# Performance work log

Hardware: AMD Instinct MI355X
Metric: run time of the kernel (lower is better)

Reference implementation:

```python
import jax, jax.numpy as jnp
import numpy as np

N = 100000
E = 6400000
H = 64  # hidden_nf


def setup_inputs() -> dict:
    key = jax.random.key(0)
    ks = jax.random.split(key, 12)
    x = jax.random.normal(ks[0], (N, 3), dtype=jnp.float32)
    vel = jax.random.normal(ks[1], (N, 3), dtype=jnp.float32)
    vel_norm = jax.random.uniform(ks[2], (N, 1), dtype=jnp.float32)
    edge_index = jax.random.randint(ks[3], (2, E), 0, N, dtype=jnp.int32)
    # coord_mlp_vel: Linear(1,H) -> LeakyReLU(0.2) -> Linear(H,1)
    W1 = jax.random.normal(ks[4], (H, 1), dtype=jnp.float32) * (1.0 / np.sqrt(1))
    b1 = jnp.zeros((H,), dtype=jnp.float32)
    W2 = jax.random.normal(ks[5], (1, H), dtype=jnp.float32) * (1.0 / np.sqrt(H))
    b2 = jnp.zeros((1,), dtype=jnp.float32)
    # phi: Linear(1,H) -> LeakyReLU(0.2) -> Linear(H,1,bias=False, xavier gain=0.001) -> Tanh
    Wp1 = jax.random.normal(ks[6], (H, 1), dtype=jnp.float32) * (1.0 / np.sqrt(1))
    bp1 = jnp.zeros((H,), dtype=jnp.float32)
    Wp2 = jax.random.normal(ks[7], (1, H), dtype=jnp.float32) * 0.001
    return {"x": x, "vel_norm": vel_norm, "vel": vel, "edge_index": edge_index,
            "W1": W1, "b1": b1, "W2": W2, "b2": b2,
            "Wp1": Wp1, "bp1": bp1, "Wp2": Wp2}


def reference(x, vel_norm, vel, edge_index, W1, b1, W2, b2, Wp1, bp1, Wp2):
    row, col = edge_index[0], edge_index[1]
    # edge_model: gather endpoint positions, radial distance -> tiny MLP -> scaled diff
    x_diff = x[row] - x[col]                                   # [E, 3]
    radial = jnp.sqrt(jnp.sum(x_diff * x_diff, axis=1, keepdims=True))  # [E, 1]
    h = jax.nn.leaky_relu(radial @ Wp1.T + bp1, 0.2)           # [E, H]
    e_out = jnp.tanh(h @ Wp2.T)                                # [E, 1]
    m_ij = x_diff * e_out                                      # [E, 3]
    # node_model: unsorted_segment_mean over row
    agg_sum = jax.ops.segment_sum(m_ij, row, num_segments=x.shape[0])           # [N, 3]
    cnt = jax.ops.segment_sum(jnp.ones((m_ij.shape[0], 1), m_ij.dtype), row,
                              num_segments=x.shape[0])                           # [N, 1]
    x_out = x + agg_sum / jnp.maximum(cnt, 1.0)
    # velocity term: x + vel * coord_mlp_vel(vel_norm)
    hv = jax.nn.leaky_relu(vel_norm @ W1.T + b1, 0.2)          # [N, H]
    scale = hv @ W2.T + b2                                     # [N, 1]
    return x_out + vel * scale
```

## Files before the change

kernel.cpp:

```cpp
#include <hip/hip_runtime.h>
#include <hip/hip_fp16.h>
#include <math.h>

#define LEAKY 0.2f
#define HDIM 64
#define EPB 4096
#define TPB1 256
#define PERT (EPB / TPB1)
#define RANGE 1024
#define RSH 10
#define KMAX 128
#define NSUB 4
#define NSLICE 8
#define FS2 262144.0f
#define INVFS2 (1.0f / 262144.0f)
#define FBIAS 4194304


__device__ __forceinline__ float fast_tanh(float v) {
    float e = __builtin_amdgcn_exp2f(v * 2.88539008178f);
    return 1.0f - 2.0f * __builtin_amdgcn_rcpf(e + 1.0f);
}

__device__ __forceinline__ float edge_eo(float rad, float C, bool slow,
                                         const float* sW1, const float* sb1,
                                         const float* sW2) {
    if (!slow) return fast_tanh(C * rad);
    float a = 0.f;
    #pragma unroll
    for (int k = 0; k < HDIM; k++) {
        float h = fmaf(rad, sW1[k], sb1[k]);
        h = (h > 0.f) ? h : LEAKY * h;
        a = fmaf(sW2[k], h, a);
    }
    return fast_tanh(a);
}

__global__ void repack_h_kernel(const float* __restrict__ x, uint2* __restrict__ xh, int N,
                                const float* __restrict__ Wp1, const float* __restrict__ bp1,
                                const float* __restrict__ Wp2, float* __restrict__ consts,
                                uint4* __restrict__ acc4, unsigned* __restrict__ cursor, int K) {
    int i = blockIdx.x * blockDim.x + threadIdx.x;
    if (i < N) {
        unsigned hx = __half_as_ushort(__float2half(x[3*i]));
        unsigned hy = __half_as_ushort(__float2half(x[3*i+1]));
        unsigned hz = __half_as_ushort(__float2half(x[3*i+2]));
        xh[i] = make_uint2((hy << 16) | hx, hz);
        acc4[i] = make_uint4(0u, 0u, 0u, 0u);
    }
    if (blockIdx.x == 0) {
        if (threadIdx.x < 64) {
            int k = threadIdx.x;
            float w1 = Wp1[k];
            float slope = (w1 >= 0.f) ? 1.f : LEAKY;
            float c = Wp2[k] * w1 * slope;
            float bnz = (bp1[k] != 0.f) ? 1.f : 0.f;
            #pragma unroll
            for (int off = 32; off > 0; off >>= 1) {
                c += __shfl_down(c, off, 64);
                bnz += __shfl_down(bnz, off, 64);
            }
            if (k == 0) { consts[0] = c; consts[1] = bnz; }
        }
        for (int k = threadIdx.x; k < NSUB * K; k += 256) cursor[k] = 0u;
    }
}

__device__ __forceinline__ unsigned long long pack_rec(float dx, float dy, float dz,
                                                       float eo, unsigned lid) {
    unsigned hx = __half_as_ushort(__float2half(dx * eo));
    unsigned hy = __half_as_ushort(__float2half(dy * eo));
    unsigned hz = __half_as_ushort(__float2half(dz * eo));
    return (unsigned long long)lid
         | ((unsigned long long)hx << 11)
         | ((unsigned long long)hy << 27)
         | ((unsigned long long)hz << 43);
}

__device__ __forceinline__ uint2 make_record(uint2 ga, uint2 gb, int r,
                                             float C, bool slow,
                                             const float* sW1, const float* sb1,
                                             const float* sW2) {
    float ax = __half2float(__ushort_as_half((unsigned short)(ga.x & 0xFFFF)));
    float ay = __half2float(__ushort_as_half((unsigned short)(ga.x >> 16)));
    float az = __half2float(__ushort_as_half((unsigned short)(ga.y & 0xFFFF)));
    float bx = __half2float(__ushort_as_half((unsigned short)(gb.x & 0xFFFF)));
    float by = __half2float(__ushort_as_half((unsigned short)(gb.x >> 16)));
    float bz = __half2float(__ushort_as_half((unsigned short)(gb.y & 0xFFFF)));
    float dx = ax - bx, dy = ay - by, dz = az - bz;
    float rad = sqrtf(dx*dx + dy*dy + dz*dz);
    float eo = edge_eo(rad, C, slow, sW1, sb1, sW2);
    unsigned long long u = pack_rec(dx, dy, dz, eo, (unsigned)r & (RANGE - 1));
    return make_uint2((unsigned)u, (unsigned)(u >> 32));
}

__device__ __forceinline__ void rec_to_acc4(uint2 r, unsigned b_, unsigned* acc4) {
    unsigned long long u = ((unsigned long long)r.y << 32) | r.x;
    unsigned lid = (unsigned)(u & (RANGE - 1));
    unsigned node = b_ * RANGE + lid;
    float mx = __half2float(__ushort_as_half((unsigned short)((u >> 11) & 0xFFFF)));
    float my = __half2float(__ushort_as_half((unsigned short)((u >> 27) & 0xFFFF)));
    float mz = __half2float(__ushort_as_half((unsigned short)((u >> 43) & 0xFFFF)));
    atomicAdd(&acc4[4*node + 0], (unsigned)__float2int_rn(mx * FS2));
    atomicAdd(&acc4[4*node + 1], (unsigned)__float2int_rn(my * FS2));
    atomicAdd(&acc4[4*node + 2], (unsigned)__float2int_rn(mz * FS2));
    atomicAdd(&acc4[4*node + 3], 1u);
}

__global__ __launch_bounds__(TPB1) void fused5_kernel(
        const uint2* __restrict__ xh,
        const int* __restrict__ ei,
        const float* __restrict__ Wp1, const float* __restrict__ bp1,
        const float* __restrict__ Wp2, const float* __restrict__ consts,
        unsigned* __restrict__ cursor, unsigned* __restrict__ acc4,
        uint2* __restrict__ recs, int E, int K, unsigned csub) {
    __shared__ uint2 stage[EPB];
    __shared__ unsigned char bucket_of[EPB];
    __shared__ unsigned hist[KMAX];
    __shared__ unsigned scanv[KMAX + 1];
    __shared__ unsigned cur[KMAX];
    __shared__ unsigned gstart[KMAX];
    __shared__ float sW1[HDIM], sb1[HDIM], sW2[HDIM];
    const float C = consts[0];
    const bool slow = (consts[1] != 0.f);
    const unsigned sub = (unsigned)blockIdx.x & (NSUB - 1);
    if (slow) {
        for (int k = threadIdx.x; k < HDIM; k += TPB1) {
            sW1[k] = Wp1[k]; sb1[k] = bp1[k]; sW2[k] = Wp2[k];
        }
    }
    for (int k = threadIdx.x; k < K; k += TPB1) hist[k] = 0;
    __syncthreads();

    const size_t base = (size_t)blockIdx.x * EPB;
    const unsigned t = threadIdx.x;
    uint2 rc[PERT];
    unsigned bk[PERT];
    if (base + EPB <= (size_t)E && (E & 3) == 0) {
        const int4* pr = (const int4*)(ei + base);
        const int4* pc = (const int4*)(ei + (size_t)E + base);
        int4 rv0 = pr[t];
        int4 rv1 = pr[t + TPB1];
        int4 rv2 = pr[t + 2 * TPB1];
        int4 rv3 = pr[t + 3 * TPB1];
        int4 cv0 = pc[t];
        int4 cv1 = pc[t + TPB1];
        int4 cv2 = pc[t + 2 * TPB1];
        int4 cv3 = pc[t + 3 * TPB1];
        {
            uint2 ga0 = xh[rv0.x], ga1 = xh[rv0.y], ga2 = xh[rv0.z], ga3 = xh[rv0.w];
            uint2 ga4 = xh[rv1.x], ga5 = xh[rv1.y], ga6 = xh[rv1.z], ga7 = xh[rv1.w];
            uint2 gb0 = xh[cv0.x], gb1 = xh[cv0.y], gb2 = xh[cv0.z], gb3 = xh[cv0.w];
            uint2 gb4 = xh[cv1.x], gb5 = xh[cv1.y], gb6 = xh[cv1.z], gb7 = xh[cv1.w];
            rc[0] = make_record(ga0, gb0, rv0.x, C, slow, sW1, sb1, sW2);
            rc[1] = make_record(ga1, gb1, rv0.y, C, slow, sW1, sb1, sW2);
            rc[2] = make_record(ga2, gb2, rv0.z, C, slow, sW1, sb1, sW2);
            rc[3] = make_record(ga3, gb3, rv0.w, C, slow, sW1, sb1, sW2);
            rc[4] = make_record(ga4, gb4, rv1.x, C, slow, sW1, sb1, sW2);
            rc[5] = make_record(ga5, gb5, rv1.y, C, slow, sW1, sb1, sW2);
            rc[6] = make_record(ga6, gb6, rv1.z, C, slow, sW1, sb1, sW2);
            rc[7] = make_record(ga7, gb7, rv1.w, C, slow, sW1, sb1, sW2);
        }
        {
            uint2 ga0 = xh[rv2.x], ga1 = xh[rv2.y], ga2 = xh[rv2.z], ga3 = xh[rv2.w];
            uint2 ga4 = xh[rv3.x], ga5 = xh[rv3.y], ga6 = xh[rv3.z], ga7 = xh[rv3.w];
            uint2 gb0 = xh[cv2.x], gb1 = xh[cv2.y], gb2 = xh[cv2.z], gb3 = xh[cv2.w];
            uint2 gb4 = xh[cv3.x], gb5 = xh[cv3.y], gb6 = xh[cv3.z], gb7 = xh[cv3.w];
            rc[8]  = make_record(ga0, gb0, rv2.x, C, slow, sW1, sb1, sW2);
            rc[9]  = make_record(ga1, gb1, rv2.y, C, slow, sW1, sb1, sW2);
            rc[10] = make_record(ga2, gb2, rv2.z, C, slow, sW1, sb1, sW2);
            rc[11] = make_record(ga3, gb3, rv2.w, C, slow, sW1, sb1, sW2);
            rc[12] = make_record(ga4, gb4, rv3.x, C, slow, sW1, sb1, sW2);
            rc[13] = make_record(ga5, gb5, rv3.y, C, slow, sW1, sb1, sW2);
            rc[14] = make_record(ga6, gb6, rv3.z, C, slow, sW1, sb1, sW2);
            rc[15] = make_record(ga7, gb7, rv3.w, C, slow, sW1, sb1, sW2);
        }
        bk[0]  = (unsigned)rv0.x >> RSH; bk[1]  = (unsigned)rv0.y >> RSH;
        bk[2]  = (unsigned)rv0.z >> RSH; bk[3]  = (unsigned)rv0.w >> RSH;
        bk[4]  = (unsigned)rv1.x >> RSH; bk[5]  = (unsigned)rv1.y >> RSH;
        bk[6]  = (unsigned)rv1.z >> RSH; bk[7]  = (unsigned)rv1.w >> RSH;
        bk[8]  = (unsigned)rv2.x >> RSH; bk[9]  = (unsigned)rv2.y >> RSH;
        bk[10] = (unsigned)rv2.z >> RSH; bk[11] = (unsigned)rv2.w >> RSH;
        bk[12] = (unsigned)rv3.x >> RSH; bk[13] = (unsigned)rv3.y >> RSH;
        bk[14] = (unsigned)rv3.z >> RSH; bk[15] = (unsigned)rv3.w >> RSH;
        #pragma unroll
        for (int i = 0; i < PERT; i++) atomicAdd(&hist[bk[i]], 1u);
    } else {
        #pragma unroll
        for (int i = 0; i < PERT; i++) {
            size_t e = base + (size_t)i * TPB1 + t;
            bk[i] = 0xFFFFFFFFu;
            if (e < (size_t)E) {
                int r = ei[e];
                int c = ei[(size_t)E + e];
                uint2 ga = xh[r], gb = xh[c];
                rc[i] = make_record(ga, gb, r, C, slow, sW1, sb1, sW2);
                bk[i] = (unsigned)r >> RSH;
                atomicAdd(&hist[bk[i]], 1u);
            }
        }
    }
    __syncthreads();
    unsigned res = 0;
    if (t < (unsigned)K) {
        unsigned myc = hist[t];
        if (myc) res = atomicAdd(&cursor[t * NSUB + sub], myc);
    }
    if (t >= 192) {
        int l = t - 192;
        unsigned origA = (l < K) ? hist[l] : 0u;
        unsigned origB = (l + 64 < K) ? hist[l + 64] : 0u;
        unsigned a = origA, b = origB;
        #pragma unroll
        for (int off = 1; off < 64; off <<= 1) {
            unsigned va = __shfl_up(a, off, 64);
            unsigned vb = __shfl_up(b, off, 64);
            if (l >= off) { a += va; b += vb; }
        }
        unsigned totA = __shfl(a, 63, 64);
        unsigned grand = totA + __shfl(b, 63, 64);
        unsigned exA = a - origA;
        unsigned exB = totA + b - origB;
        scanv[l] = exA;  cur[l] = exA;
        scanv[l + 64] = exB;  cur[l + 64] = exB;
        if (l == 63) scanv[K] = grand;
    }
    __syncthreads();
    #pragma unroll
    for (int i = 0; i < PERT; i++) {
        if (bk[i] != 0xFFFFFFFFu) {
            unsigned slot = atomicAdd(&cur[bk[i]], 1u);
            stage[slot] = rc[i];
            bucket_of[slot] = (unsigned char)bk[i];
        }
    }
    if (t < (unsigned)K) gstart[t] = res;
    __syncthreads();
    unsigned total = scanv[K];
    for (unsigned j = t; j < total; j += TPB1) {
        unsigned b_ = bucket_of[j];
        unsigned off = gstart[b_] + (j - scanv[b_]);
        if (off < csub) recs[(size_t)(b_ * NSUB + sub) * csub + off] = stage[j];
        else            rec_to_acc4(stage[j], b_, acc4);
    }
}

__device__ __forceinline__ void proc_rec2(unsigned lo, unsigned hi,
                                          unsigned long long* accA,
                                          unsigned long long* accB) {
    unsigned long long u = ((unsigned long long)hi << 32) | lo;
    unsigned lid = (unsigned)(u & (RANGE - 1));
    float mx = __half2float(__ushort_as_half((unsigned short)((u >> 11) & 0xFFFF)));
    float my = __half2float(__ushort_as_half((unsigned short)((u >> 27) & 0xFFFF)));
    float mz = __half2float(__ushort_as_half((unsigned short)((u >> 43) & 0xFFFF)));
    unsigned ix = (unsigned)(__float2int_rn(mx * FS2) + FBIAS);
    unsigned iy = (unsigned)(__float2int_rn(my * FS2) + FBIAS);
    unsigned iz = (unsigned)(__float2int_rn(mz * FS2) + FBIAS);
    atomicAdd(&accA[lid], ((unsigned long long)ix << 32) | (unsigned long long)iy);
    atomicAdd(&accB[lid], ((unsigned long long)iz << 32) | 1ull);
}

__global__ __launch_bounds__(256) void reduce5_kernel(
        const uint2* __restrict__ recs, const unsigned* __restrict__ cursor,
        uint4* __restrict__ slices, int N, int K, unsigned csub) {
    __shared__ unsigned long long accA[RANGE];
    __shared__ unsigned long long accB[RANGE];
    const int b = blockIdx.x / NSLICE;
    const int s = blockIdx.x % NSLICE;
    const int r = s & (NSUB - 1);
    const int p = s / NSUB;
    for (int i = threadIdx.x; i < RANGE; i += 256) { accA[i] = 0ull; accB[i] = 0ull; }
    __syncthreads();
    unsigned cnt = cursor[b * NSUB + r];
    if (cnt > csub) cnt = csub;
    unsigned pairs = (cnt + 1) >> 1;
    unsigned perp = (pairs + 1) >> 1;
    unsigned p0 = (unsigned)p * perp;
    unsigned p1 = p0 + perp; if (p1 > pairs) p1 = pairs;
    const uint4* rb4 = (const uint4*)(recs + (size_t)(b * NSUB + r) * csub);
    unsigned j = p0 + threadIdx.x;
    if (p0 < p1) {
        while (j + 256 < p1) {
            uint4 v0 = rb4[j];
            uint4 v1 = rb4[j + 256];
            proc_rec2(v0.x, v0.y, accA, accB);
            if (2*j + 1 < cnt) proc_rec2(v0.z, v0.w, accA, accB);
            proc_rec2(v1.x, v1.y, accA, accB);
            if (2*(j+256) + 1 < cnt) proc_rec2(v1.z, v1.w, accA, accB);
            j += 512;
        }
        while (j < p1) {
            uint4 v = rb4[j];
            proc_rec2(v.x, v.y, accA, accB);
            if (2*j + 1 < cnt) proc_rec2(v.z, v.w, accA, accB);
            j += 256;
        }
    }
    __syncthreads();
    const int nbase = b * RANGE;
    for (int i = threadIdx.x; i < RANGE; i += 256) {
        int node = nbase + i;
        if (node < N) {
            unsigned long long A = accA[i], B = accB[i];
            slices[(size_t)s * N + node] =
                make_uint4((unsigned)(A >> 32), (unsigned)A,
                           (unsigned)(B >> 32), (unsigned)B);
        }
    }
}

__global__ void node_merge_kernel(const float* __restrict__ x,
                                  const float* __restrict__ vel_norm,
                                  const float* __restrict__ vel,
                                  const float* __restrict__ W1, const float* __restrict__ b1,
                                  const float* __restrict__ W2, const float* __restrict__ b2,
                                  const uint4* __restrict__ slices,
                                  const uint4* __restrict__ acc4,
                                  float* __restrict__ out, int N) {
    __shared__ float sW1[HDIM], sb1[HDIM], sW2[HDIM];
    for (int k = threadIdx.x; k < HDIM; k += blockDim.x) {
        sW1[k] = W1[k]; sb1[k] = b1[k]; sW2[k] = W2[k];
    }
    __syncthreads();
    int i = blockIdx.x * blockDim.x + threadIdx.x;
    if (i >= N) return;
    unsigned long long sxb = 0, syb = 0, szb = 0;
    unsigned sc = 0;
    #pragma unroll
    for (int s = 0; s < NSLICE; s++) {
        uint4 v = slices[(size_t)s * N + i];
        sxb += v.x; syb += v.y; szb += v.z; sc += v.w;
    }
    uint4 a4 = acc4[i];
    long long fx = (long long)sxb - (long long)sc * (long long)FBIAS + (long long)(int)a4.x;
    long long fy = (long long)syb - (long long)sc * (long long)FBIAS + (long long)(int)a4.y;
    long long fz = (long long)szb - (long long)sc * (long long)FBIAS + (long long)(int)a4.z;
    float cntf = (float)(sc + a4.w);
    float sx = (float)fx * INVFS2;
    float sy = (float)fy * INVFS2;
    float sz = (float)fz * INVFS2;
    float vn = vel_norm[i];
    float a = b2[0];
    #pragma unroll
    for (int k = 0; k < HDIM; k++) {
        float h = fmaf(vn, sW1[k], sb1[k]);
        h = (h > 0.f) ? h : LEAKY * h;
        a = fmaf(sW2[k], h, a);
    }
    float inv = 1.0f / fmaxf(cntf, 1.0f);
    out[3*i]     = x[3*i]     + sx * inv + vel[3*i]     * a;
    out[3*i + 1] = x[3*i + 1] + sy * inv + vel[3*i + 1] * a;
    out[3*i + 2] = x[3*i + 2] + sz * inv + vel[3*i + 2] * a;
}

__global__ void precompute_kernel(const float* __restrict__ Wp1,
                                  const float* __restrict__ bp1,
                                  const float* __restrict__ Wp2,
                                  float* __restrict__ consts) {
    int k = threadIdx.x;
    float w1 = Wp1[k];
    float slope = (w1 >= 0.f) ? 1.f : LEAKY;
    float c = Wp2[k] * w1 * slope;
    float bnz = (bp1[k] != 0.f) ? 1.f : 0.f;
    #pragma unroll
    for (int off = 32; off > 0; off >>= 1) {
        c += __shfl_down(c, off, 64);
        bnz += __shfl_down(bnz, off, 64);
    }
    if (k == 0) { consts[0] = c; consts[1] = bnz; }
}

__global__ void edge_atomic_kernel(const float* __restrict__ x, const int* __restrict__ ei,
                                   const float* __restrict__ Wp1, const float* __restrict__ bp1,
                                   const float* __restrict__ Wp2, const float* __restrict__ consts,
                                   float* __restrict__ acc, int E) {
    __shared__ float sW1[HDIM], sb1[HDIM], sW2[HDIM];
    const float C = consts[0];
    const bool slow = (consts[1] != 0.f);
    if (slow) {
        for (int k = threadIdx.x; k < HDIM; k += blockDim.x) {
            sW1[k] = Wp1[k]; sb1[k] = bp1[k]; sW2[k] = Wp2[k];
        }
        __syncthreads();
    }
    int e = blockIdx.x * blockDim.x + threadIdx.x;
    if (e >= E) return;
    int r = ei[e];
    int c = ei[E + e];
    float dx = x[3*r] - x[3*c];
    float dy = x[3*r+1] - x[3*c+1];
    float dz = x[3*r+2] - x[3*c+2];
    float rad = sqrtf(dx*dx + dy*dy + dz*dz);
    float eo = edge_eo(rad, C, slow, sW1, sb1, sW2);
    float* basep = acc + ((size_t)r << 2);
    atomicAdd(basep + 0, dx * eo);
    atomicAdd(basep + 1, dy * eo);
    atomicAdd(basep + 2, dz * eo);
    atomicAdd(basep + 3, 1.f);
}

__global__ void node_kernel(const float* __restrict__ x, const float* __restrict__ vel_norm,
                            const float* __restrict__ vel,
                            const float* __restrict__ W1, const float* __restrict__ b1,
                            const float* __restrict__ W2, const float* __restrict__ b2,
                            const float4* __restrict__ slices,
                            float* __restrict__ out, int N, int S) {
    __shared__ float sW1[HDIM], sb1[HDIM], sW2[HDIM];
    for (int k = threadIdx.x; k < HDIM; k += blockDim.x) {
        sW1[k] = W1[k]; sb1[k] = b1[k]; sW2[k] = W2[k];
    }
    __syncthreads();
    int i = blockIdx.x * blockDim.x + threadIdx.x;
    if (i >= N) return;
    float sx = 0.f, sy = 0.f, sz = 0.f, sc = 0.f;
    for (int s = 0; s < S; s++) {
        float4 v = slices[(size_t)s * N + i];
        sx += v.x; sy += v.y; sz += v.z; sc += v.w;
    }
    float vn = vel_norm[i];
    float a = b2[0];
    #pragma unroll
    for (int k = 0; k < HDIM; k++) {
        float h = fmaf(vn, sW1[k], sb1[k]);
        h = (h > 0.f) ? h : LEAKY * h;
        a = fmaf(sW2[k], h, a);
    }
    float inv = 1.0f / fmaxf(sc, 1.0f);
    out[3*i]     = x[3*i]     + sx * inv + vel[3*i]     * a;
    out[3*i + 1] = x[3*i + 1] + sy * inv + vel[3*i + 1] * a;
    out[3*i + 2] = x[3*i + 2] + sz * inv + vel[3*i + 2] * a;
}

extern "C" void kernel_launch(void* const* d_in, const int* in_sizes, int n_in,
                              void* d_out, int out_size, void* d_ws, size_t ws_size,
                              hipStream_t stream) {
    const float* x        = (const float*)d_in[0];
    const float* vel_norm = (const float*)d_in[1];
    const float* vel      = (const float*)d_in[2];
    const int*   ei       = (const int*)  d_in[3];
    const float* W1       = (const float*)d_in[4];
    const float* b1       = (const float*)d_in[5];
    const float* W2       = (const float*)d_in[6];
    const float* b2       = (const float*)d_in[7];
    const float* Wp1      = (const float*)d_in[8];
    const float* bp1      = (const float*)d_in[9];
    const float* Wp2      = (const float*)d_in[10];

    const int N = in_sizes[0] / 3;
    const int E = in_sizes[3] / 2;
    const int K = (N + RANGE - 1) / RANGE;
    const int nblk = (E + EPB - 1) / EPB;

    unsigned csub = (unsigned)(E / (K * NSUB)) + 1024u;
    csub = (csub + 63u) & ~63u;

    size_t rec_bytes = (size_t)K * NSUB * csub * sizeof(uint2);
    size_t sp_slices = rec_bytes;
    size_t sp_xh     = sp_slices + (size_t)NSLICE * N * sizeof(uint4);
    size_t sp_acc    = (sp_xh + (size_t)N * sizeof(uint2) + 15) & ~(size_t)15;
    size_t sp_cur    = sp_acc + (size_t)N * sizeof(uint4);
    size_t sp_const  = (sp_cur + (size_t)NSUB * KMAX * sizeof(unsigned) + 15) & ~(size_t)15;
    size_t need      = sp_const + 32;

    if (K <= KMAX && ws_size >= need) {
        uint2*    recs   = (uint2*)   d_ws;
        uint4*    slices = (uint4*)   ((char*)d_ws + sp_slices);
        uint2*    xh     = (uint2*)   ((char*)d_ws + sp_xh);
        unsigned* acc4   = (unsigned*)((char*)d_ws + sp_acc);
        unsigned* cursor = (unsigned*)((char*)d_ws + sp_cur);
        float*    consts = (float*)   ((char*)d_ws + sp_const);

        repack_h_kernel<<<(N + 255) / 256, 256, 0, stream>>>(
            x, xh, N, Wp1, bp1, Wp2, consts, (uint4*)acc4, cursor, K);
        fused5_kernel<<<nblk, TPB1, 0, stream>>>(
            xh, ei, Wp1, bp1, Wp2, consts, cursor, acc4, recs, E, K, csub);
        reduce5_kernel<<<K * NSLICE, 256, 0, stream>>>(recs, cursor, slices, N, K, csub);
        node_merge_kernel<<<(N + 255) / 256, 256, 0, stream>>>(
            x, vel_norm, vel, W1, b1, W2, b2, slices, (const uint4*)acc4,
            (float*)d_out, N);
    } else {
        float* acc    = (float*)d_ws;
        float* consts = (float*)((char*)d_ws + (size_t)N * sizeof(float4));
        hipMemsetAsync(d_ws, 0, (size_t)N * sizeof(float4) + 32, stream);
        precompute_kernel<<<1, 64, 0, stream>>>(Wp1, bp1, Wp2, consts);
        edge_atomic_kernel<<<(E + 255) / 256, 256, 0, stream>>>(x, ei, Wp1, bp1, Wp2,
                                                                consts, acc, E);
        node_kernel<<<(N + 255) / 256, 256, 0, stream>>>(x, vel_norm, vel, W1, b1, W2, b2,
                                                         (const float4*)acc, (float*)d_out, N, 1);
    }
}
```

Before: 185.8 us.

## Scatter edge records directly to global buckets, dropping LDS staging and scan

New measurement: 198.3 us. 6.7% more time.

```diff
diff --git a/kernel.cpp b/kernel.cpp
--- a/kernel.cpp
+++ b/kernel.cpp
@@ -4,7 +4,7 @@
 
 #define LEAKY 0.2f
 #define HDIM 64
-#define EPB 4096
+#define EPB 2048
 #define TPB1 256
 #define PERT (EPB / TPB1)
 #define RANGE 1024
@@ -107,18 +107,15 @@
     atomicAdd(&acc4[4*node + 3], 1u);
 }
 
-__global__ __launch_bounds__(TPB1) void fused5_kernel(
+__global__ __launch_bounds__(TPB1, 6) void fused6_kernel(
         const uint2* __restrict__ xh,
         const int* __restrict__ ei,
         const float* __restrict__ Wp1, const float* __restrict__ bp1,
         const float* __restrict__ Wp2, const float* __restrict__ consts,
         unsigned* __restrict__ cursor, unsigned* __restrict__ acc4,
         uint2* __restrict__ recs, int E, int K, unsigned csub) {
-    __shared__ uint2 stage[EPB];
-    __shared__ unsigned char bucket_of[EPB];
     __shared__ unsigned hist[KMAX];
-    __shared__ unsigned scanv[KMAX + 1];
-    __shared__ unsigned cur[KMAX];
+    __shared__ unsigned curk[KMAX];
     __shared__ unsigned gstart[KMAX];
     __shared__ float sW1[HDIM], sb1[HDIM], sW2[HDIM];
     const float C = consts[0];
@@ -129,7 +126,7 @@
             sW1[k] = Wp1[k]; sb1[k] = bp1[k]; sW2[k] = Wp2[k];
         }
     }
-    for (int k = threadIdx.x; k < K; k += TPB1) hist[k] = 0;
+    for (int k = threadIdx.x; k < K; k += TPB1) { hist[k] = 0; curk[k] = 0; }
     __syncthreads();
 
     const size_t base = (size_t)blockIdx.x * EPB;
@@ -141,48 +138,24 @@
         const int4* pc = (const int4*)(ei + (size_t)E + base);
         int4 rv0 = pr[t];
         int4 rv1 = pr[t + TPB1];
-        int4 rv2 = pr[t + 2 * TPB1];
-        int4 rv3 = pr[t + 3 * TPB1];
         int4 cv0 = pc[t];
         int4 cv1 = pc[t + TPB1];
-        int4 cv2 = pc[t + 2 * TPB1];
-        int4 cv3 = pc[t + 3 * TPB1];
-        {
-            uint2 ga0 = xh[rv0.x], ga1 = xh[rv0.y], ga2 = xh[rv0.z], ga3 = xh[rv0.w];
-            uint2 ga4 = xh[rv1.x], ga5 = xh[rv1.y], ga6 = xh[rv1.z], ga7 = xh[rv1.w];
-            uint2 gb0 = xh[cv0.x], gb1 = xh[cv0.y], gb2 = xh[cv0.z], gb3 = xh[cv0.w];
-            uint2 gb4 = xh[cv1.x], gb5 = xh[cv1.y], gb6 = xh[cv1.z], gb7 = xh[cv1.w];
-            rc[0] = make_record(ga0, gb0, rv0.x, C, slow, sW1, sb1, sW2);
-            rc[1] = make_record(ga1, gb1, rv0.y, C, slow, sW1, sb1, sW2);
-            rc[2] = make_record(ga2, gb2, rv0.z, C, slow, sW1, sb1, sW2);
-            rc[3] = make_record(ga3, gb3, rv0.w, C, slow, sW1, sb1, sW2);
-            rc[4] = make_record(ga4, gb4, rv1.x, C, slow, sW1, sb1, sW2);
-            rc[5] = make_record(ga5, gb5, rv1.y, C, slow, sW1, sb1, sW2);
-            rc[6] = make_record(ga6, gb6, rv1.z, C, slow, sW1, sb1, sW2);
-            rc[7] = make_record(ga7, gb7, rv1.w, C, slow, sW1, sb1, sW2);
-        }
-        {
-            uint2 ga0 = xh[rv2.x], ga1 = xh[rv2.y], ga2 = xh[rv2.z], ga3 = xh[rv2.w];
-            uint2 ga4 = xh[rv3.x], ga5 = xh[rv3.y], ga6 = xh[rv3.z], ga7 = xh[rv3.w];
-            uint2 gb0 = xh[cv2.x], gb1 = xh[cv2.y], gb2 = xh[cv2.z], gb3 = xh[cv2.w];
-            uint2 gb4 = xh[cv3.x], gb5 = xh[cv3.y], gb6 = xh[cv3.z], gb7 = xh[cv3.w];
-            rc[8]  = make_record(ga0, gb0, rv2.x, C, slow, sW1, sb1, sW2);
-            rc[9]  = make_record(ga1, gb1, rv2.y, C, slow, sW1, sb1, sW2);
-            rc[10] = make_record(ga2, gb2, rv2.z, C, slow, sW1, sb1, sW2);
-            rc[11] = make_record(ga3, gb3, rv2.w, C, slow, sW1, sb1, sW2);
-            rc[12] = make_record(ga4, gb4, rv3.x, C, slow, sW1, sb1, sW2);
-            rc[13] = make_record(ga5, gb5, rv3.y, C, slow, sW1, sb1, sW2);
-            rc[14] = make_record(ga6, gb6, rv3.z, C, slow, sW1, sb1, sW2);
-            rc[15] = make_record(ga7, gb7, rv3.w, C, slow, sW1, sb1, sW2);
-        }
-        bk[0]  = (unsigned)rv0.x >> RSH; bk[1]  = (unsigned)rv0.y >> RSH;
-        bk[2]  = (unsigned)rv0.z >> RSH; bk[3]  = (unsigned)rv0.w >> RSH;
-        bk[4]  = (unsigned)rv1.x >> RSH; bk[5]  = (unsigned)rv1.y >> RSH;
-        bk[6]  = (unsigned)rv1.z >> RSH; bk[7]  = (unsigned)rv1.w >> RSH;
-        bk[8]  = (unsigned)rv2.x >> RSH; bk[9]  = (unsigned)rv2.y >> RSH;
-        bk[10] = (unsigned)rv2.z >> RSH; bk[11] = (unsigned)rv2.w >> RSH;
-        bk[12] = (unsigned)rv3.x >> RSH; bk[13] = (unsigned)rv3.y >> RSH;
-        bk[14] = (unsigned)rv3.z >> RSH; bk[15] = (unsigned)rv3.w >> RSH;
+        uint2 ga0 = xh[rv0.x], ga1 = xh[rv0.y], ga2 = xh[rv0.z], ga3 = xh[rv0.w];
+        uint2 ga4 = xh[rv1.x], ga5 = xh[rv1.y], ga6 = xh[rv1.z], ga7 = xh[rv1.w];
+        uint2 gb0 = xh[cv0.x], gb1 = xh[cv0.y], gb2 = xh[cv0.z], gb3 = xh[cv0.w];
+        uint2 gb4 = xh[cv1.x], gb5 = xh[cv1.y], gb6 = xh[cv1.z], gb7 = xh[cv1.w];
+        rc[0] = make_record(ga0, gb0, rv0.x, C, slow, sW1, sb1, sW2);
+        rc[1] = make_record(ga1, gb1, rv0.y, C, slow, sW1, sb1, sW2);
+        rc[2] = make_record(ga2, gb2, rv0.z, C, slow, sW1, sb1, sW2);
+        rc[3] = make_record(ga3, gb3, rv0.w, C, slow, sW1, sb1, sW2);
+        rc[4] = make_record(ga4, gb4, rv1.x, C, slow, sW1, sb1, sW2);
+        rc[5] = make_record(ga5, gb5, rv1.y, C, slow, sW1, sb1, sW2);
+        rc[6] = make_record(ga6, gb6, rv1.z, C, slow, sW1, sb1, sW2);
+        rc[7] = make_record(ga7, gb7, rv1.w, C, slow, sW1, sb1, sW2);
+        bk[0] = (unsigned)rv0.x >> RSH; bk[1] = (unsigned)rv0.y >> RSH;
+        bk[2] = (unsigned)rv0.z >> RSH; bk[3] = (unsigned)rv0.w >> RSH;
+        bk[4] = (unsigned)rv1.x >> RSH; bk[5] = (unsigned)rv1.y >> RSH;
+        bk[6] = (unsigned)rv1.z >> RSH; bk[7] = (unsigned)rv1.w >> RSH;
         #pragma unroll
         for (int i = 0; i < PERT; i++) atomicAdd(&hist[bk[i]], 1u);
     } else {
@@ -201,47 +174,19 @@
         }
     }
     __syncthreads();
-    unsigned res = 0;
     if (t < (unsigned)K) {
         unsigned myc = hist[t];
-        if (myc) res = atomicAdd(&cursor[t * NSUB + sub], myc);
-    }
-    if (t >= 192) {
-        int l = t - 192;
-        unsigned origA = (l < K) ? hist[l] : 0u;
-        unsigned origB = (l + 64 < K) ? hist[l + 64] : 0u;
-        unsigned a = origA, b = origB;
-        #pragma unroll
-        for (int off = 1; off < 64; off <<= 1) {
-            unsigned va = __shfl_up(a, off, 64);
-            unsigned vb = __shfl_up(b, off, 64);
-            if (l >= off) { a += va; b += vb; }
-        }
-        unsigned totA = __shfl(a, 63, 64);
-        unsigned grand = totA + __shfl(b, 63, 64);
-        unsigned exA = a - origA;
-        unsigned exB = totA + b - origB;
-        scanv[l] = exA;  cur[l] = exA;
-        scanv[l + 64] = exB;  cur[l + 64] = exB;
-        if (l == 63) scanv[K] = grand;
+        gstart[t] = myc ? atomicAdd(&cursor[t * NSUB + sub], myc) : 0u;
     }
     __syncthreads();
     #pragma unroll
     for (int i = 0; i < PERT; i++) {
         if (bk[i] != 0xFFFFFFFFu) {
-            unsigned slot = atomicAdd(&cur[bk[i]], 1u);
-            stage[slot] = rc[i];
-            bucket_of[slot] = (unsigned char)bk[i];
-        }
-    }
-    if (t < (unsigned)K) gstart[t] = res;
-    __syncthreads();
-    unsigned total = scanv[K];
-    for (unsigned j = t; j < total; j += TPB1) {
-        unsigned b_ = bucket_of[j];
-        unsigned off = gstart[b_] + (j - scanv[b_]);
-        if (off < csub) recs[(size_t)(b_ * NSUB + sub) * csub + off] = stage[j];
-        else            rec_to_acc4(stage[j], b_, acc4);
+            unsigned r = atomicAdd(&curk[bk[i]], 1u);
+            unsigned off = gstart[bk[i]] + r;
+            if (off < csub) recs[(size_t)(bk[i] * NSUB + sub) * csub + off] = rc[i];
+            else            rec_to_acc4(rc[i], bk[i], acc4);
+        }
     }
 }
 
@@ -472,7 +417,7 @@
 
         repack_h_kernel<<<(N + 255) / 256, 256, 0, stream>>>(
             x, xh, N, Wp1, bp1, Wp2, consts, (uint4*)acc4, cursor, K);
-        fused5_kernel<<<nblk, TPB1, 0, stream>>>(
+        fused6_kernel<<<nblk, TPB1, 0, stream>>>(
             xh, ei, Wp1, bp1, Wp2, consts, cursor, acc4, recs, E, K, csub);
         reduce5_kernel<<<K * NSLICE, 256, 0, stream>>>(recs, cursor, slices, N, K, csub);
         node_merge_kernel<<<(N + 255) / 256, 256, 0, stream>>>(
```

## Fuse segment reduction with node update into one kernel per range

Applied to the files above, without the earlier changes.

After: 186.9 us. Within noise of the previous version (+0.6%).

```diff
diff --git a/kernel.cpp b/kernel.cpp
--- a/kernel.cpp
+++ b/kernel.cpp
@@ -11,7 +11,6 @@
 #define RSH 10
 #define KMAX 128
 #define NSUB 4
-#define NSLICE 8
 #define FS2 262144.0f
 #define INVFS2 (1.0f / 262144.0f)
 #define FBIAS 4194304
@@ -260,97 +259,65 @@
     atomicAdd(&accB[lid], ((unsigned long long)iz << 32) | 1ull);
 }
 
-__global__ __launch_bounds__(256) void reduce5_kernel(
+__global__ __launch_bounds__(1024) void reduce_node_kernel(
         const uint2* __restrict__ recs, const unsigned* __restrict__ cursor,
-        uint4* __restrict__ slices, int N, int K, unsigned csub) {
+        const float* __restrict__ x, const float* __restrict__ vel_norm,
+        const float* __restrict__ vel,
+        const float* __restrict__ W1, const float* __restrict__ b1,
+        const float* __restrict__ W2, const float* __restrict__ b2,
+        const uint4* __restrict__ acc4,
+        float* __restrict__ out, int N, unsigned csub) {
     __shared__ unsigned long long accA[RANGE];
     __shared__ unsigned long long accB[RANGE];
-    const int b = blockIdx.x / NSLICE;
-    const int s = blockIdx.x % NSLICE;
-    const int r = s & (NSUB - 1);
-    const int p = s / NSUB;
-    for (int i = threadIdx.x; i < RANGE; i += 256) { accA[i] = 0ull; accB[i] = 0ull; }
-    __syncthreads();
-    unsigned cnt = cursor[b * NSUB + r];
-    if (cnt > csub) cnt = csub;
-    unsigned pairs = (cnt + 1) >> 1;
-    unsigned perp = (pairs + 1) >> 1;
-    unsigned p0 = (unsigned)p * perp;
-    unsigned p1 = p0 + perp; if (p1 > pairs) p1 = pairs;
-    const uint4* rb4 = (const uint4*)(recs + (size_t)(b * NSUB + r) * csub);
-    unsigned j = p0 + threadIdx.x;
-    if (p0 < p1) {
-        while (j + 256 < p1) {
-            uint4 v0 = rb4[j];
-            uint4 v1 = rb4[j + 256];
-            proc_rec2(v0.x, v0.y, accA, accB);
-            if (2*j + 1 < cnt) proc_rec2(v0.z, v0.w, accA, accB);
-            proc_rec2(v1.x, v1.y, accA, accB);
-            if (2*(j+256) + 1 < cnt) proc_rec2(v1.z, v1.w, accA, accB);
-            j += 512;
-        }
-        while (j < p1) {
+    __shared__ float sW1[HDIM], sb1[HDIM], sW2[HDIM];
+    const int b = blockIdx.x;
+    const unsigned t = threadIdx.x;
+    if (t < HDIM) { sW1[t] = W1[t]; sb1[t] = b1[t]; sW2[t] = W2[t]; }
+    accA[t] = 0ull; accB[t] = 0ull;
+    __syncthreads();
+    #pragma unroll
+    for (int r = 0; r < NSUB; r++) {
+        unsigned cnt = cursor[b * NSUB + r];
+        if (cnt > csub) cnt = csub;
+        const uint2* rb = recs + (size_t)(b * NSUB + r) * csub;
+        const uint4* rb4 = (const uint4*)rb;
+        unsigned pairs = cnt >> 1;
+        for (unsigned j = t; j < pairs; j += 1024) {
             uint4 v = rb4[j];
             proc_rec2(v.x, v.y, accA, accB);
-            if (2*j + 1 < cnt) proc_rec2(v.z, v.w, accA, accB);
-            j += 256;
-        }
-    }
-    __syncthreads();
-    const int nbase = b * RANGE;
-    for (int i = threadIdx.x; i < RANGE; i += 256) {
-        int node = nbase + i;
-        if (node < N) {
-            unsigned long long A = accA[i], B = accB[i];
-            slices[(size_t)s * N + node] =
-                make_uint4((unsigned)(A >> 32), (unsigned)A,
-                           (unsigned)(B >> 32), (unsigned)B);
-        }
-    }
-}
-
-__global__ void node_merge_kernel(const float* __restrict__ x,
-                                  const float* __restrict__ vel_norm,
-                                  const float* __restrict__ vel,
-                                  const float* __restrict__ W1, const float* __restrict__ b1,
-                                  const float* __restrict__ W2, const float* __restrict__ b2,
-                                  const uint4* __restrict__ slices,
-                                  const uint4* __restrict__ acc4,
-                                  float* __restrict__ out, int N) {
-    __shared__ float sW1[HDIM], sb1[HDIM], sW2[HDIM];
-    for (int k = threadIdx.x; k < HDIM; k += blockDim.x) {
-        sW1[k] = W1[k]; sb1[k] = b1[k]; sW2[k] = W2[k];
-    }
-    __syncthreads();
-    int i = blockIdx.x * blockDim.x + threadIdx.x;
-    if (i >= N) return;
-    unsigned long long sxb = 0, syb = 0, szb = 0;
-    unsigned sc = 0;
-    #pragma unroll
-    for (int s = 0; s < NSLICE; s++) {
-        uint4 v = slices[(size_t)s * N + i];
-        sxb += v.x; syb += v.y; szb += v.z; sc += v.w;
-    }
-    uint4 a4 = acc4[i];
-    long long fx = (long long)sxb - (long long)sc * (long long)FBIAS + (long long)(int)a4.x;
-    long long fy = (long long)syb - (long long)sc * (long long)FBIAS + (long long)(int)a4.y;
-    long long fz = (long long)szb - (long long)sc * (long long)FBIAS + (long long)(int)a4.z;
-    float cntf = (float)(sc + a4.w);
-    float sx = (float)fx * INVFS2;
-    float sy = (float)fy * INVFS2;
-    float sz = (float)fz * INVFS2;
-    float vn = vel_norm[i];
-    float a = b2[0];
-    #pragma unroll
-    for (int k = 0; k < HDIM; k++) {
-        float h = fmaf(vn, sW1[k], sb1[k]);
-        h = (h > 0.f) ? h : LEAKY * h;
-        a = fmaf(sW2[k], h, a);
-    }
-    float inv = 1.0f / fmaxf(cntf, 1.0f);
-    out[3*i]     = x[3*i]     + sx * inv + vel[3*i]     * a;
-    out[3*i + 1] = x[3*i + 1] + sy * inv + vel[3*i + 1] * a;
-    out[3*i + 2] = x[3*i + 2] + sz * inv + vel[3*i + 2] * a;
+            proc_rec2(v.z, v.w, accA, accB);
+        }
+        if ((cnt & 1u) && t == 0) {
+            uint2 last = rb[cnt - 1];
+            proc_rec2(last.x, last.y, accA, accB);
+        }
+    }
+    __syncthreads();
+    int node = b * RANGE + (int)t;
+    if (node < N) {
+        unsigned long long A = accA[t], B = accB[t];
+        unsigned sc = (unsigned)B;
+        uint4 a4 = acc4[node];
+        long long fx = (long long)(A >> 32) - (long long)sc * (long long)FBIAS + (long long)(int)a4.x;
+        long long fy = (long long)(unsigned)A - (long long)sc * (long long)FBIAS + (long long)(int)a4.y;
+        long long fz = (long long)(B >> 32) - (long long)sc * (long long)FBIAS + (long long)(int)a4.z;
+        float cntf = (float)(sc + a4.w);
+        float sx = (float)fx * INVFS2;
+        float sy = (float)fy * INVFS2;
+        float sz = (float)fz * INVFS2;
+        float vn = vel_norm[node];
+        float a = b2[0];
+        #pragma unroll
+        for (int k = 0; k < HDIM; k++) {
+            float h = fmaf(vn, sW1[k], sb1[k]);
+            h = (h > 0.f) ? h : LEAKY * h;
+            a = fmaf(sW2[k], h, a);
+        }
+        float inv = 1.0f / fmaxf(cntf, 1.0f);
+        out[3*node]     = x[3*node]     + sx * inv + vel[3*node]     * a;
+        out[3*node + 1] = x[3*node + 1] + sy * inv + vel[3*node + 1] * a;
+        out[3*node + 2] = x[3*node + 2] + sz * inv + vel[3*node + 2] * a;
+    }
 }
 
 __global__ void precompute_kernel(const float* __restrict__ Wp1,
@@ -455,8 +422,7 @@
     csub = (csub + 63u) & ~63u;
 
     size_t rec_bytes = (size_t)K * NSUB * csub * sizeof(uint2);
-    size_t sp_slices = rec_bytes;
-    size_t sp_xh     = sp_slices + (size_t)NSLICE * N * sizeof(uint4);
+    size_t sp_xh     = rec_bytes;
     size_t sp_acc    = (sp_xh + (size_t)N * sizeof(uint2) + 15) & ~(size_t)15;
     size_t sp_cur    = sp_acc + (size_t)N * sizeof(uint4);
     size_t sp_const  = (sp_cur + (size_t)NSUB * KMAX * sizeof(unsigned) + 15) & ~(size_t)15;
@@ -464,7 +430,6 @@
 
     if (K <= KMAX && ws_size >= need) {
         uint2*    recs   = (uint2*)   d_ws;
-        uint4*    slices = (uint4*)   ((char*)d_ws + sp_slices);
         uint2*    xh     = (uint2*)   ((char*)d_ws + sp_xh);
         unsigned* acc4   = (unsigned*)((char*)d_ws + sp_acc);
         unsigned* cursor = (unsigned*)((char*)d_ws + sp_cur);
@@ -474,10 +439,9 @@
             x, xh, N, Wp1, bp1, Wp2, consts, (uint4*)acc4, cursor, K);
         fused5_kernel<<<nblk, TPB1, 0, stream>>>(
             xh, ei, Wp1, bp1, Wp2, consts, cursor, acc4, recs, E, K, csub);
-        reduce5_kernel<<<K * NSLICE, 256, 0, stream>>>(recs, cursor, slices, N, K, csub);
-        node_merge_kernel<<<(N + 255) / 256, 256, 0, stream>>>(
-            x, vel_norm, vel, W1, b1, W2, b2, slices, (const uint4*)acc4,
-            (float*)d_out, N);
+        reduce_node_kernel<<<K, 1024, 0, stream>>>(
+            recs, cursor, x, vel_norm, vel, W1, b1, W2, b2,
+            (const uint4*)acc4, (float*)d_out, N, csub);
     } else {
         float* acc    = (float*)d_ws;
         float* consts = (float*)((char*)d_ws + (size_t)N * sizeof(float4));
```
